# Kernel tuning notes

Hardware: AMD Instinct MI355X
Metric: run time of the kernel (lower is better)

The kernel has to match this reference:

```python
import jax, jax.numpy as jnp
import numpy as np

P = 4          # patch_size
LAM = 0.5      # init_lambda
B, C, H, W = 8, 96, 128, 128

def _dct_mat(N):
    # torch_dct unnormalized DCT-II matrix: D[k,n] = 2*cos(pi*(2n+1)k/(2N))
    n = np.arange(N)
    return 2.0 * np.cos(np.pi * (2.0 * n[None, :] + 1.0) * n[:, None] / (2.0 * N))

_D = jnp.asarray(_dct_mat(P), dtype=jnp.float32)
_Di = jnp.asarray(np.linalg.inv(_dct_mat(P)), dtype=jnp.float32)  # exact inverse -> idct(dct(x)) == x

def _dct2(x):
    # DCT-II over last two dims of [..., P, P]
    return jnp.einsum('ij,...jk,lk->...il', _D, x, _D)

def _idct2(x):
    return jnp.einsum('ij,...jk,lk->...il', _Di, x, _Di)

def _conv3x3(x, w, b):
    y = jax.lax.conv_general_dilated(x, w, (1, 1), 'SAME',
                                     dimension_numbers=('NCHW', 'OIHW', 'NCHW'))
    return y + b[None, :, None, None]

def setup_inputs() -> dict:
    key = jax.random.key(0)
    ks = jax.random.split(key, 5)
    std = 1.0 / np.sqrt(C * 9)
    return {
        'input1': jax.random.normal(ks[0], (B, C, H, W), jnp.float32),
        'input2': jax.random.normal(ks[1], (B, C, H, W), jnp.float32),
        'wq': jax.random.normal(ks[2], (C, C, 3, 3), jnp.float32) * std,
        'bq': jnp.zeros((C,), jnp.float32),
        'wk': jax.random.normal(ks[3], (C, C, 3, 3), jnp.float32) * std,
        'bk': jnp.zeros((C,), jnp.float32),
        'wv': jax.random.normal(ks[4], (C, C, 3, 3), jnp.float32) * std,
        'bv': jnp.zeros((C,), jnp.float32),
        'temperature': jnp.ones((1, 1), jnp.float32),
    }

def reference(input1, input2, wq, bq, wk, bk, wv, bv, temperature):
    b, c, h, w = input1.shape
    F_Q = _conv3x3(input1, wq, bq)
    F_K = _conv3x3(input1, wk, bk)
    F_V = _conv3x3(input2, wv, bv)
    hp, wp = h // P, w // P
    # 'b c (h p1) (w p2) -> b c h w p1 p2'
    to_patch = lambda x: x.reshape(b, c, hp, P, wp, P).transpose(0, 1, 2, 4, 3, 5)
    fft_Q = _dct2(to_patch(F_Q))          # [b,c,hp,wp,P,P]
    fft_K = _dct2(to_patch(F_K))
    F1 = jnp.matmul(fft_Q, fft_K)         # per-patch PxP matmul
    L = hp * wp * P * P                   # == h*w
    F1f = F1.reshape(b, c, L)
    Fq = fft_Q.reshape(b, c, L)
    Fk = fft_K.reshape(b, c, L)
    # channel-channel attention: [b,c,L] @ [b,L,c] -> [b,c,c]
    attn = jnp.einsum('bil,bjl->bij', Fq, Fk) * temperature[0, 0]
    attn = jax.nn.softmax(attn, axis=-1)
    Fcfr = jnp.einsum('bij,bjl->bil', attn, F1f).reshape(b, c, hp, wp, P, P)
    Fcfr_out = _idct2(Fcfr)
    # 'b c h w p1 p2 -> b c (h p1) (w p2)'
    Fcfrout = Fcfr_out.transpose(0, 1, 2, 4, 3, 5).reshape(b, c, h, w)
    out1 = jnp.matmul(Fcfrout, F_V)       # batched HxW matmul (H==W)
    Fdfr = F_V - out1 * LAM
    return jnp.matmul(Fcfrout, F_Q) + Fdfr
```

## Files before the change

### kernel.cpp

```cpp
#include <hip/hip_runtime.h>

typedef unsigned short u16;
typedef unsigned int u32;
typedef __bf16 bf16x8 __attribute__((ext_vector_type(8)));
typedef float f32x4 __attribute__((ext_vector_type(4)));
typedef int i32x4 __attribute__((ext_vector_type(4)));

#define BATCH 8
#define CH 96
#define HWSZ 16384
#define PADP (130*130*96)

#define OFF_FQ     0ULL
#define OFF_FK     50331648ULL
#define OFF_GT     50331648ULL
#define OFF_FVN    75497472ULL
#define OFF_PAD1H  100663296ULL
#define OFF_F1W    100663296ULL
#define OFF_PART   126621696ULL
#define OFF_PAD1L  126621696ULL
#define OFF_PAD2   152580096ULL
#define OFF_FCFR   152580096ULL
#define OFF_FVB    178538496ULL
#define OFF_ATTNB  203704320ULL
#define OFF_WQK    203851776ULL
#define OFF_WV     204515328ULL
#define WS_NEED    204681216ULL

__device__ __forceinline__ u16 f2bf(float f) {
    u32 u = __builtin_bit_cast(u32, f);
    u += 0x7fffu + ((u >> 16) & 1u);
    return (u16)(u >> 16);
}
__device__ __forceinline__ float bf2f(u16 h) {
    u32 u = ((u32)h) << 16;
    return __builtin_bit_cast(float, u);
}
__device__ __forceinline__ f32x4 mfma16(i32x4 a, i32x4 b, f32x4 c) {
    return __builtin_amdgcn_mfma_f32_16x16x32_bf16(
        __builtin_bit_cast(bf16x8, a), __builtin_bit_cast(bf16x8, b), c, 0, 0, 0);
}
__device__ __forceinline__ void gl_lds16(const u16* g, u16* l) {
    __builtin_amdgcn_global_load_lds(
        (const __attribute__((address_space(1))) unsigned int*)g,
        (__attribute__((address_space(3))) unsigned int*)l, 16, 0, 0);
}

__global__ __launch_bounds__(256) void k_diag(float* __restrict__ out, int n, float val) {
    for (int i = blockIdx.x * 256 + threadIdx.x; i < n; i += gridDim.x * 256) out[i] = val;
}

__global__ __launch_bounds__(256) void k_zhalo(u16* __restrict__ p) {
    size_t base = (size_t)blockIdx.x * PADP;
    for (int i = threadIdx.x; i < 130 * 96; i += 256) {
        p[base + i] = 0;
        p[base + (size_t)129 * 130 * 96 + i] = 0;
    }
    for (int i = threadIdx.x; i < 128 * 2 * 96; i += 256) {
        int row = i / 192, k = i - row * 192;
        int x = (k < 96) ? 0 : 129, c = (k < 96) ? k : k - 96;
        p[base + ((size_t)(row + 1) * 130 + x) * 96 + c] = 0;
    }
}

__global__ __launch_bounds__(256) void k_trans_split(const float* __restrict__ src,
        u16* __restrict__ dh, u16* __restrict__ dl) {
    __shared__ float tile[96][129];
    int b = blockIdx.x >> 7, y = blockIdx.x & 127;
    const float* s = src + (size_t)b * CH * HWSZ + (size_t)y * 128;
    for (int idx = threadIdx.x; idx < CH * 128; idx += 256) {
        int c = idx >> 7, x = idx & 127;
        tile[c][x] = s[(size_t)c * HWSZ + x];
    }
    __syncthreads();
    size_t obase = ((size_t)(b * 130 + y + 1) * 130 + 1) * 96;
    for (int idx = threadIdx.x; idx < 128 * CH; idx += 256) {
        int x = idx / CH, c = idx - x * CH;
        float v = tile[c][x];
        u16 h = f2bf(v);
        dh[obase + idx] = h;
        if (dl) dl[obase + idx] = f2bf(v - bf2f(h));
    }
}

__global__ __launch_bounds__(128) void k_weights_all(const float* __restrict__ wq,
        const float* __restrict__ wk, const float* __restrict__ wv,
        u16* __restrict__ dqk, u16* __restrict__ dv) {
    int co = blockIdx.x;
    if (co < 192) {
        const float* w = (co < 96) ? wq : wk;
        int cs = (co < 96) ? co : co - 96;
        for (int idx = threadIdx.x; idx < 864; idx += 128) {
            int tap = idx / 96, ci = idx - tap * 96;
            int cic = ci >> 5, g = (ci >> 3) & 3, c7 = ci & 7;
            float v = w[((size_t)cs * 96 + ci) * 9 + tap];
            u16 h = f2bf(v), lo = f2bf(v - bf2f(h));
            size_t s = (size_t)(cic * 9 + tap);
            dqk[(((s * 2 + 0) * 4 + g) * 192 + co) * 8 + c7] = h;
            dqk[(((s * 2 + 1) * 4 + g) * 192 + co) * 8 + c7] = lo;
        }
    } else {
        int cs = co - 192;
        for (int idx = threadIdx.x; idx < 864; idx += 128) {
            int tap = idx / 96, ci = idx - tap * 96;
            int cic = ci >> 5, g = (ci >> 3) & 3, c7 = ci & 7;
            float v = wv[((size_t)cs * 96 + ci) * 9 + tap];
            size_t s = (size_t)(cic * 9 + tap);
            dv[((s * 4 + g) * 96 + cs) * 8 + c7] = f2bf(v);
        }
    }
}

__global__ __launch_bounds__(512, 4) void k_convqk6(
        const u16* __restrict__ ph, const u16* __restrict__ pl,
        const u16* __restrict__ wqk,
        const float* __restrict__ bq, const float* __restrict__ bk,
        float* __restrict__ fq, float* __restrict__ fk) {
    __shared__ u16 wbuf[2][12288];
    const int tid = threadIdx.x;
    const int wg = ((blockIdx.x & 7) << 7) | (blockIdx.x >> 3);
    const int b = wg >> 7, y = wg & 127;
    const int w = tid >> 6, lane = tid & 63, l15 = lane & 15, g = lane >> 4;
    const int wx = w & 3, wc = w >> 2;
    f32x4 acc[2][6];
#pragma unroll
    for (int mf = 0; mf < 2; mf++)
#pragma unroll
        for (int f = 0; f < 6; f++) acc[mf][f] = (f32x4){0.f, 0.f, 0.f, 0.f};

    {
#pragma unroll
        for (int j = 0; j < 3; j++)
            gl_lds16(wqk + (size_t)(tid + j * 512) * 8, &wbuf[0][(size_t)(tid + j * 512) * 8]);
    }
    i32x4 ah0, ah1, al0, al1;
    {
        size_t ab = ((size_t)(b * 130 + y) * 130 + (wx * 32 + l15)) * 96 + g * 8;
        ah0 = *(const i32x4*)(ph + ab);
        ah1 = *(const i32x4*)(ph + ab + 16 * 96);
        al0 = *(const i32x4*)(pl + ab);
        al1 = *(const i32x4*)(pl + ab + 16 * 96);
    }
    __syncthreads();
    for (int s = 0; s < 27; s++) {
        const int cur = s & 1;
        i32x4 nh0, nh1, nl0, nl1;
        if (s + 1 < 27) {
            const u16* src = wqk + (size_t)(s + 1) * 12288;
#pragma unroll
            for (int j = 0; j < 3; j++)
                gl_lds16(src + (size_t)(tid + j * 512) * 8, &wbuf[cur ^ 1][(size_t)(tid + j * 512) * 8]);
            const int s1 = s + 1;
            const int cic1 = s1 / 9, tap1 = s1 - cic1 * 9;
            const int dy1 = tap1 / 3 - 1, dx1 = tap1 - (tap1 / 3) * 3 - 1;
            size_t ab = ((size_t)(b * 130 + y + 1 + dy1) * 130 + (wx * 32 + l15 + 1 + dx1)) * 96
                      + cic1 * 32 + g * 8;
            nh0 = *(const i32x4*)(ph + ab);
            nh1 = *(const i32x4*)(ph + ab + 16 * 96);
            nl0 = *(const i32x4*)(pl + ab);
            nl1 = *(const i32x4*)(pl + ab + 16 * 96);
        }
#pragma unroll
        for (int f = 0; f < 6; f++) {
            const int cob = wc * 96 + f * 16 + l15;
            i32x4 bh = *(const i32x4*)(&wbuf[cur][((0 + g) * 192 + cob) * 8]);
            i32x4 bl = *(const i32x4*)(&wbuf[cur][((4 + g) * 192 + cob) * 8]);
            acc[0][f] = mfma16(ah0, bh, acc[0][f]);
            acc[0][f] = mfma16(ah0, bl, acc[0][f]);
            acc[0][f] = mfma16(al0, bh, acc[0][f]);
            acc[1][f] = mfma16(ah1, bh, acc[1][f]);
            acc[1][f] = mfma16(ah1, bl, acc[1][f]);
            acc[1][f] = mfma16(al1, bh, acc[1][f]);
        }
        __syncthreads();
        if (s + 1 < 27) { ah0 = nh0; ah1 = nh1; al0 = nl0; al1 = nl1; }
    }
    const float* bias = wc ? bk : bq;
    float* op = wc ? fk : fq;
#pragma unroll
    for (int f = 0; f < 6; f++) {
        const int co = f * 16 + l15;
        const float bb = bias[co];
#pragma unroll
        for (int mf = 0; mf < 2; mf++) {
            const int xp = wx * 32 + mf * 16 + g * 4;
#pragma unroll
            for (int r = 0; r < 4; r++)
                op[((size_t)((b * 128 + y) * 128 + xp + r)) * 96 + co] = acc[mf][f][r] + bb;
        }
    }
}

__global__ __launch_bounds__(512, 4) void k_convv6(
        const u16* __restrict__ p2, const u16* __restrict__ wv,
        const float* __restrict__ bv, u16* __restrict__ fvb) {
    __shared__ u16 vbuf[2][3072];
    const int tid = threadIdx.x;
    const int wg = ((blockIdx.x & 7) << 7) | (blockIdx.x >> 3);
    const int b = wg >> 7, y = wg & 127;
    const int w = tid >> 6, lane = tid & 63, l15 = lane & 15, g = lane >> 4;
    const int wx = w & 3, wc = w >> 2;
    f32x4 acc[2][3];
#pragma unroll
    for (int mf = 0; mf < 2; mf++)
#pragma unroll
        for (int f = 0; f < 3; f++) acc[mf][f] = (f32x4){0.f, 0.f, 0.f, 0.f};
    if (tid < 384)
        gl_lds16(wv + (size_t)tid * 8, &vbuf[0][(size_t)tid * 8]);
    i32x4 ah0, ah1;
    {
        size_t ab = ((size_t)(b * 130 + y) * 130 + (wx * 32 + l15)) * 96 + g * 8;
        ah0 = *(const i32x4*)(p2 + ab);
        ah1 = *(const i32x4*)(p2 + ab + 16 * 96);
    }
    __syncthreads();
    for (int s = 0; s < 27; s++) {
        const int cur = s & 1;
        i32x4 nh0, nh1;
        if (s + 1 < 27) {
            if (tid < 384)
                gl_lds16(wv + (size_t)(s + 1) * 3072 + (size_t)tid * 8, &vbuf[cur ^ 1][(size_t)tid * 8]);
            const int s1 = s + 1;
            const int cic1 = s1 / 9, tap1 = s1 - cic1 * 9;
            const int dy1 = tap1 / 3 - 1, dx1 = tap1 - (tap1 / 3) * 3 - 1;
            size_t ab = ((size_t)(b * 130 + y + 1 + dy1) * 130 + (wx * 32 + l15 + 1 + dx1)) * 96
                      + cic1 * 32 + g * 8;
            nh0 = *(const i32x4*)(p2 + ab);
            nh1 = *(const i32x4*)(p2 + ab + 16 * 96);
        }
#pragma unroll
        for (int f = 0; f < 3; f++) {
            const int cof = wc * 48 + f * 16 + l15;
            i32x4 bfr = *(const i32x4*)(&vbuf[cur][(g * 96 + cof) * 8]);
            acc[0][f] = mfma16(ah0, bfr, acc[0][f]);
            acc[1][f] = mfma16(ah1, bfr, acc[1][f]);
        }
        __syncthreads();
        if (s + 1 < 27) { ah0 = nh0; ah1 = nh1; }
    }
#pragma unroll
    for (int f = 0; f < 3; f++) {
        const int co = wc * 48 + f * 16 + l15;
        const float bb = bv[co];
#pragma unroll
        for (int mf = 0; mf < 2; mf++) {
            const int xp = wx * 32 + mf * 16 + g * 4;
#pragma unroll
            for (int r = 0; r < 4; r++)
                fvb[((size_t)((b * 128 + y) * 128 + xp + r)) * 96 + co] = f2bf(acc[mf][f][r] + bb);
        }
    }
}

__global__ __launch_bounds__(256) void k_pattn(
        const float* __restrict__ fq, const float* __restrict__ fk,
        u16* __restrict__ f1w, float* __restrict__ part) {
    __shared__ float qs[96 * 129];
    __shared__ float ks[96 * 129];
    int blk = blockIdx.x;
    int b = blk >> 7, ys = (blk >> 2) & 31, xq = blk & 3;
    int y0 = ys * 4, x0 = xq * 32;
    for (int idx = threadIdx.x; idx < 3072; idx += 256) {
        int p = idx / 24, c0 = (idx - p * 24) * 4;
        int ry = p >> 5, rx = p & 31;
        size_t off = ((size_t)((b * 128 + y0 + ry) * 128 + x0 + rx)) * 96 + c0;
        f32x4 qv = *(const f32x4*)(fq + off);
        f32x4 kv = *(const f32x4*)(fk + off);
#pragma unroll
        for (int u = 0; u < 4; u++) {
            qs[(c0 + u) * 129 + p] = qv[u];
            ks[(c0 + u) * 129 + p] = kv[u];
        }
    }
    __syncthreads();
#pragma unroll
    for (int it = 0; it < 3; it++) {
        int item = threadIdx.x + it * 256;
        int j = item / 96, c = item - j * 96;
        float A[4][4], Bm[4][4];
#pragma unroll
        for (int r = 0; r < 4; r++)
#pragma unroll
            for (int m = 0; m < 4; m++) {
                A[r][m] = qs[c * 129 + r * 32 + j * 4 + m];
                Bm[r][m] = ks[c * 129 + r * 32 + j * 4 + m];
            }
        float rsB[4], csB[4], rsA[4], tot = 0.f;
#pragma unroll
        for (int r = 0; r < 4; r++) {
            rsB[r] = Bm[r][0] + Bm[r][1] + Bm[r][2] + Bm[r][3];
            rsA[r] = A[r][0] + A[r][1] + A[r][2] + A[r][3];
            tot += rsB[r];
        }
#pragma unroll
        for (int m = 0; m < 4; m++) csB[m] = Bm[0][m] + Bm[1][m] + Bm[2][m] + Bm[3][m];
#pragma unroll
        for (int r = 0; r < 4; r++)
#pragma unroll
            for (int m = 0; m < 4; m++) {
                float ab = A[r][0] * Bm[0][m] + A[r][1] * Bm[1][m]
                         + A[r][2] * Bm[2][m] + A[r][3] * Bm[3][m];
                f1w[((size_t)((b * 128 + y0 + r) * 128 + x0 + j * 4 + m)) * 96 + c]
                    = f2bf(8.f * ab + 2.f * rsA[r] * csB[m]);
            }
#pragma unroll
        for (int r = 0; r < 4; r++)
#pragma unroll
            for (int m = 0; m < 4; m++)
                ks[c * 129 + r * 32 + j * 4 + m]
                    = 64.f * Bm[r][m] + 16.f * (rsB[r] + csB[m]) + 4.f * tot;
    }
    __syncthreads();
    int tx = threadIdx.x & 15, ty = threadIdx.x >> 4;
    double accD[6][6];
#pragma unroll
    for (int a = 0; a < 6; a++)
#pragma unroll
        for (int bb = 0; bb < 6; bb++) accD[a][bb] = 0.0;
#pragma unroll
    for (int ch = 0; ch < 2; ch++) {
        float acc[6][6];
#pragma unroll
        for (int a = 0; a < 6; a++)
#pragma unroll
            for (int bb = 0; bb < 6; bb++) acc[a][bb] = 0.f;
        for (int l = ch * 64; l < ch * 64 + 64; l++) {
            float qv[6], kv[6];
#pragma unroll
            for (int a = 0; a < 6; a++) qv[a] = qs[(ty + 16 * a) * 129 + l];
#pragma unroll
            for (int bb = 0; bb < 6; bb++) kv[bb] = ks[(tx + 16 * bb) * 129 + l];
#pragma unroll
            for (int a = 0; a < 6; a++)
#pragma unroll
                for (int bb = 0; bb < 6; bb++) acc[a][bb] += qv[a] * kv[bb];
        }
#pragma unroll
        for (int a = 0; a < 6; a++)
#pragma unroll
            for (int bb = 0; bb < 6; bb++) accD[a][bb] += (double)acc[a][bb];
    }
    int s128 = ys * 4 + xq;
#pragma unroll
    for (int a = 0; a < 6; a++)
#pragma unroll
        for (int bb = 0; bb < 6; bb++)
            part[((size_t)((b * 128 + s128) * 96 + ty + 16 * a)) * 96 + tx + 16 * bb]
                = (float)accD[a][bb];
}

__global__ __launch_bounds__(128) void k_softmax(
        const float* __restrict__ part, const float* __restrict__ temp,
        u16* __restrict__ attnb) {
    __shared__ float red[128];
    int b = blockIdx.x / 96, i2 = blockIdx.x - b * 96;
    int j2 = threadIdx.x;
    float v = 0.f;
    if (j2 < 96) {
        double vd = 0.0;
        for (int s = 0; s < 128; s++)
            vd += (double)part[((size_t)((b * 128 + s) * 96 + i2)) * 96 + j2];
        v = (float)vd * temp[0];
    }
    red[j2] = (j2 < 96) ? v : -3.4e38f;
    __syncthreads();
    for (int off = 64; off >= 1; off >>= 1) {
        if (j2 < off) red[j2] = fmaxf(red[j2], red[j2 + off]);
        __syncthreads();
    }
    float mx = red[0];
    __syncthreads();
    float e = (j2 < 96) ? expf(v - mx) : 0.f;
    red[j2] = e;
    __syncthreads();
    for (int off = 64; off >= 1; off >>= 1) {
        if (j2 < off) red[j2] += red[j2 + off];
        __syncthreads();
    }
    float sum = red[0];
    if (j2 < 96) attnb[((size_t)(b * 96) + i2) * 96 + j2] = f2bf(e / sum);
}

__global__ __launch_bounds__(256) void k_gprep(
        const float* __restrict__ fqn, const u16* __restrict__ fvb,
        u16* __restrict__ gt, u16* __restrict__ fvn) {
    __shared__ u16 lg[8 * 32 * 33];
    __shared__ u16 lv[8 * 32 * 33];
    int blk = blockIdx.x;
    int b = blk / 192;
    int r = blk - b * 192;
    int yt = r / 48; r -= yt * 48;
    int xt = r / 12; int cc = r - xt * 12;
    int y0 = yt * 32, x0 = xt * 32, c0 = cc * 8;
    for (int idx = threadIdx.x; idx < 8192; idx += 256) {
        int pix = idx >> 3, cl = idx & 7;
        int yy = pix >> 5, xx = pix & 31;
        size_t off = ((size_t)((b * 128 + y0 + yy) * 128 + x0 + xx)) * 96 + c0 + cl;
        float q = fqn[off];
        float v = bf2f(fvb[off]);
        int la = (cl * 32 + yy) * 33 + xx;
        lg[la] = f2bf(q - 0.5f * v);
        lv[la] = f2bf(v);
    }
    __syncthreads();
    for (int idx = threadIdx.x; idx < 8192; idx += 256) {
        int yy = idx & 31, xl = (idx >> 5) & 31, cl = idx >> 10;
        gt[((size_t)((b * 96 + c0 + cl) * 128 + x0 + xl)) * 128 + y0 + yy] = lg[(cl * 32 + yy) * 33 + xl];
    }
    for (int idx = threadIdx.x; idx < 8192; idx += 256) {
        int xx = idx & 31, yl = (idx >> 5) & 31, cl = idx >> 10;
        fvn[((size_t)((b * 96 + c0 + cl) * 128 + y0 + yl)) * 128 + x0 + xx] = lv[(cl * 32 + yl) * 33 + xx];
    }
}

__global__ __launch_bounds__(256) void k_fcfr2(
        const u16* __restrict__ attnb, const u16* __restrict__ f1w,
        u16* __restrict__ fc) {
    int b = blockIdx.x >> 6, pc = blockIdx.x & 63;
    int lane = threadIdx.x & 63, wv_ = threadIdx.x >> 6;
    int l15 = lane & 15, g = lane >> 4;
    int pbase = pc * 256 + wv_ * 64;
    f32x4 acc[6][4];
#pragma unroll
    for (int m = 0; m < 6; m++)
#pragma unroll
        for (int n = 0; n < 4; n++) acc[m][n] = (f32x4){0.f, 0.f, 0.f, 0.f};
#pragma unroll
    for (int ks = 0; ks < 3; ks++) {
        int k0 = ks * 32 + g * 8;
        i32x4 afr[6];
#pragma unroll
        for (int m = 0; m < 6; m++)
            afr[m] = *(const i32x4*)(attnb + ((size_t)(b * 96 + m * 16 + l15)) * 96 + k0);
#pragma unroll
        for (int n = 0; n < 4; n++) {
            i32x4 bfr = *(const i32x4*)(f1w + ((size_t)(b * 16384 + pbase + n * 16 + l15)) * 96 + k0);
#pragma unroll
            for (int m = 0; m < 6; m++)
                acc[m][n] = mfma16(afr[m], bfr, acc[m][n]);
        }
    }
#pragma unroll
    for (int m = 0; m < 6; m++)
#pragma unroll
        for (int n = 0; n < 4; n++)
#pragma unroll
            for (int r = 0; r < 4; r++) {
                int i2 = m * 16 + g * 4 + r;
                int pix = pbase + n * 16 + l15;
                fc[((size_t)(b * 96 + i2)) * HWSZ + pix] = f2bf(acc[m][n][r]);
            }
}

__global__ __launch_bounds__(256) void k_final(
        const u16* __restrict__ fc, const u16* __restrict__ gt,
        const u16* __restrict__ fvn, float* __restrict__ out) {
    int b = blockIdx.x / 96, c = blockIdx.x - b * 96;
    int lane = threadIdx.x & 63, wv_ = threadIdx.x >> 6;
    int l15 = lane & 15, g = lane >> 4;
    const u16* A = fc + ((size_t)(b * 96 + c)) * HWSZ;
    const u16* Bm = gt + ((size_t)(b * 96 + c)) * HWSZ;
    f32x4 acc[2][8];
#pragma unroll
    for (int mf = 0; mf < 2; mf++)
#pragma unroll
        for (int nf = 0; nf < 8; nf++) acc[mf][nf] = (f32x4){0.f, 0.f, 0.f, 0.f};
#pragma unroll
    for (int kc = 0; kc < 4; kc++) {
        int k0 = kc * 32 + g * 8;
        i32x4 af[2];
#pragma unroll
        for (int mf = 0; mf < 2; mf++)
            af[mf] = *(const i32x4*)(A + (size_t)(wv_ * 32 + mf * 16 + l15) * 128 + k0);
#pragma unroll
        for (int nf = 0; nf < 8; nf++) {
            i32x4 bf = *(const i32x4*)(Bm + (size_t)(nf * 16 + l15) * 128 + k0);
#pragma unroll
            for (int mf = 0; mf < 2; mf++)
                acc[mf][nf] = mfma16(af[mf], bf, acc[mf][nf]);
        }
    }
    const u16* V = fvn + ((size_t)(b * 96 + c)) * HWSZ;
    float* O = out + ((size_t)(b * 96 + c)) * HWSZ;
#pragma unroll
    for (int mf = 0; mf < 2; mf++)
#pragma unroll
        for (int nf = 0; nf < 8; nf++)
#pragma unroll
            for (int r = 0; r < 4; r++) {
                int y = wv_ * 32 + mf * 16 + g * 4 + r;
                int x = nf * 16 + l15;
                O[y * 128 + x] = acc[mf][nf][r] + bf2f(V[y * 128 + x]);
            }
}

extern "C" void kernel_launch(void* const* d_in, const int* in_sizes, int n_in,
                              void* d_out, int out_size, void* d_ws, size_t ws_size,
                              hipStream_t stream) {
    (void)in_sizes; (void)n_in;
    if (ws_size < (size_t)WS_NEED) {
        k_diag<<<2048, 256, 0, stream>>>((float*)d_out, out_size, (float)(ws_size >> 10));
        return;
    }
    const float* in1 = (const float*)d_in[0];
    const float* in2 = (const float*)d_in[1];
    const float* wq  = (const float*)d_in[2];
    const float* bq  = (const float*)d_in[3];
    const float* wk  = (const float*)d_in[4];
    const float* bk  = (const float*)d_in[5];
    const float* wv  = (const float*)d_in[6];
    const float* bv  = (const float*)d_in[7];
    const float* temp = (const float*)d_in[8];
    char* ws = (char*)d_ws;
    float* FQ   = (float*)(ws + OFF_FQ);
    float* FK   = (float*)(ws + OFF_FK);
    u16*  GT    = (u16*)(ws + OFF_GT);
    u16*  FVN   = (u16*)(ws + OFF_FVN);
    u16*  PAD1H = (u16*)(ws + OFF_PAD1H);
    u16*  PAD1L = (u16*)(ws + OFF_PAD1L);
    u16*  PAD2  = (u16*)(ws + OFF_PAD2);
    u16*  F1W   = (u16*)(ws + OFF_F1W);
    float* PART = (float*)(ws + OFF_PART);
    u16*  FCFR  = (u16*)(ws + OFF_FCFR);
    u16*  FVB   = (u16*)(ws + OFF_FVB);
    u16*  ATTNB = (u16*)(ws + OFF_ATTNB);
    u16*  WQK   = (u16*)(ws + OFF_WQK);
    u16*  WV    = (u16*)(ws + OFF_WV);

    k_zhalo<<<24, 256, 0, stream>>>(PAD1H);
    k_trans_split<<<1024, 256, 0, stream>>>(in1, PAD1H, PAD1L);
    k_trans_split<<<1024, 256, 0, stream>>>(in2, PAD2, nullptr);
    k_weights_all<<<288, 128, 0, stream>>>(wq, wk, wv, WQK, WV);
    k_convqk6<<<1024, 512, 0, stream>>>(PAD1H, PAD1L, WQK, bq, bk, FQ, FK);
    k_convv6<<<1024, 512, 0, stream>>>(PAD2, WV, bv, FVB);
    k_pattn<<<1024, 256, 0, stream>>>(FQ, FK, F1W, PART);
    k_softmax<<<768, 128, 0, stream>>>(PART, temp, ATTNB);
    k_gprep<<<1536, 256, 0, stream>>>(FQ, FVB, GT, FVN);
    k_fcfr2<<<512, 256, 0, stream>>>(ATTNB, F1W, FCFR);
    k_final<<<768, 256, 0, stream>>>(FCFR, GT, FVN, (float*)d_out);
}
```

Before: 409.7 us.

## Split QK conv across two kernel variants and halve pattn shared memory

The Q/K convolution is split into two launches over batch halves. The first half keeps the old wave tiling; the second uses a new variant where each wave covers 64 pixels by 48 output channels, reusing each weight fragment across four M-fragments. The patch-attention kernel now stages its 128-pixel tile in two 64-pixel chunks, roughly halving LDS use so more blocks can be resident, at the cost of extra barriers. Splitting the conv looks like an A/B comparison of the two tilings, and it adds a launch plus more register pressure in the new variant.

```diff
diff --git a/kernel.cpp b/kernel.cpp
--- a/kernel.cpp
+++ b/kernel.cpp
@@ -111,15 +111,15 @@
     }
 }
 
-__global__ __launch_bounds__(512, 4) void k_convqk6(
+__global__ __launch_bounds__(512, 4) void k_convqk6h(
         const u16* __restrict__ ph, const u16* __restrict__ pl,
         const u16* __restrict__ wqk,
         const float* __restrict__ bq, const float* __restrict__ bk,
-        float* __restrict__ fq, float* __restrict__ fk) {
+        float* __restrict__ fq, float* __restrict__ fk, int bbase) {
     __shared__ u16 wbuf[2][12288];
     const int tid = threadIdx.x;
-    const int wg = ((blockIdx.x & 7) << 7) | (blockIdx.x >> 3);
-    const int b = wg >> 7, y = wg & 127;
+    const int wg = ((blockIdx.x & 7) << 6) | (blockIdx.x >> 3);
+    const int b = bbase + (wg >> 7), y = wg & 127;
     const int w = tid >> 6, lane = tid & 63, l15 = lane & 15, g = lane >> 4;
     const int wx = w & 3, wc = w >> 2;
     f32x4 acc[2][6];
@@ -127,7 +127,6 @@
     for (int mf = 0; mf < 2; mf++)
 #pragma unroll
         for (int f = 0; f < 6; f++) acc[mf][f] = (f32x4){0.f, 0.f, 0.f, 0.f};
-
     {
 #pragma unroll
         for (int j = 0; j < 3; j++)
@@ -184,6 +183,91 @@
 #pragma unroll
         for (int mf = 0; mf < 2; mf++) {
             const int xp = wx * 32 + mf * 16 + g * 4;
+#pragma unroll
+            for (int r = 0; r < 4; r++)
+                op[((size_t)((b * 128 + y) * 128 + xp + r)) * 96 + co] = acc[mf][f][r] + bb;
+        }
+    }
+}
+
+__global__ __launch_bounds__(512, 4) void k_convqk7h(
+        const u16* __restrict__ ph, const u16* __restrict__ pl,
+        const u16* __restrict__ wqk,
+        const float* __restrict__ bq, const float* __restrict__ bk,
+        float* __restrict__ fq, float* __restrict__ fk, int bbase) {
+    __shared__ u16 wbuf[2][12288];
+    const int tid = threadIdx.x;
+    const int wg = ((blockIdx.x & 7) << 6) | (blockIdx.x >> 3);
+    const int b = bbase + (wg >> 7), y = wg & 127;
+    const int w = tid >> 6, lane = tid & 63, l15 = lane & 15, g = lane >> 4;
+    const int qk = w >> 2, coh = (w >> 1) & 1, xh = w & 1;
+    const int cob = qk * 96 + coh * 48;
+    f32x4 acc[4][3];
+#pragma unroll
+    for (int mf = 0; mf < 4; mf++)
+#pragma unroll
+        for (int f = 0; f < 3; f++) acc[mf][f] = (f32x4){0.f, 0.f, 0.f, 0.f};
+    {
+#pragma unroll
+        for (int j = 0; j < 3; j++)
+            gl_lds16(wqk + (size_t)(tid + j * 512) * 8, &wbuf[0][(size_t)(tid + j * 512) * 8]);
+    }
+    i32x4 ah[4], al[4];
+    {
+        size_t ab = ((size_t)(b * 130 + y) * 130 + (xh * 64 + l15)) * 96 + g * 8;
+#pragma unroll
+        for (int mf = 0; mf < 4; mf++) {
+            ah[mf] = *(const i32x4*)(ph + ab + (size_t)mf * 16 * 96);
+            al[mf] = *(const i32x4*)(pl + ab + (size_t)mf * 16 * 96);
+        }
+    }
+    __syncthreads();
+    for (int s = 0; s < 27; s++) {
+        const int cur = s & 1;
+        i32x4 nah[4], nal[4];
+        if (s + 1 < 27) {
+            const u16* src = wqk + (size_t)(s + 1) * 12288;
+#pragma unroll
+            for (int j = 0; j < 3; j++)
+                gl_lds16(src + (size_t)(tid + j * 512) * 8, &wbuf[cur ^ 1][(size_t)(tid + j * 512) * 8]);
+            const int s1 = s + 1;
+            const int cic1 = s1 / 9, tap1 = s1 - cic1 * 9;
+            const int dy1 = tap1 / 3 - 1, dx1 = tap1 - (tap1 / 3) * 3 - 1;
+            size_t ab1 = ((size_t)(b * 130 + y + 1 + dy1) * 130 + (xh * 64 + l15 + 1 + dx1)) * 96
+                       + cic1 * 32 + g * 8;
+#pragma unroll
+            for (int mf = 0; mf < 4; mf++) {
+                nah[mf] = *(const i32x4*)(ph + ab1 + (size_t)mf * 16 * 96);
+                nal[mf] = *(const i32x4*)(pl + ab1 + (size_t)mf * 16 * 96);
+            }
+        }
+#pragma unroll
+        for (int f = 0; f < 3; f++) {
+            const int cw = cob + f * 16 + l15;
+            i32x4 bh = *(const i32x4*)(&wbuf[cur][((0 + g) * 192 + cw) * 8]);
+            i32x4 bl = *(const i32x4*)(&wbuf[cur][((4 + g) * 192 + cw) * 8]);
+#pragma unroll
+            for (int mf = 0; mf < 4; mf++) {
+                acc[mf][f] = mfma16(ah[mf], bh, acc[mf][f]);
+                acc[mf][f] = mfma16(ah[mf], bl, acc[mf][f]);
+                acc[mf][f] = mfma16(al[mf], bh, acc[mf][f]);
+            }
+        }
+        __syncthreads();
+        if (s + 1 < 27) {
+#pragma unroll
+            for (int mf = 0; mf < 4; mf++) { ah[mf] = nah[mf]; al[mf] = nal[mf]; }
+        }
+    }
+    const float* bias = qk ? bk : bq;
+    float* op = qk ? fk : fq;
+#pragma unroll
+    for (int f = 0; f < 3; f++) {
+        const int co = coh * 48 + f * 16 + l15;
+        const float bb = bias[co];
+#pragma unroll
+        for (int mf = 0; mf < 4; mf++) {
+            const int xp = xh * 64 + mf * 16 + g * 4;
 #pragma unroll
             for (int r = 0; r < 4; r++)
                 op[((size_t)((b * 128 + y) * 128 + xp + r)) * 96 + co] = acc[mf][f][r] + bb;
@@ -252,65 +336,14 @@
     }
 }
 
-__global__ __launch_bounds__(256) void k_pattn(
+__global__ __launch_bounds__(256) void k_pattn2(
         const float* __restrict__ fq, const float* __restrict__ fk,
         u16* __restrict__ f1w, float* __restrict__ part) {
-    __shared__ float qs[96 * 129];
-    __shared__ float ks[96 * 129];
+    __shared__ float qs[96 * 65];
+    __shared__ float ks[96 * 65];
     int blk = blockIdx.x;
     int b = blk >> 7, ys = (blk >> 2) & 31, xq = blk & 3;
     int y0 = ys * 4, x0 = xq * 32;
-    for (int idx = threadIdx.x; idx < 3072; idx += 256) {
-        int p = idx / 24, c0 = (idx - p * 24) * 4;
-        int ry = p >> 5, rx = p & 31;
-        size_t off = ((size_t)((b * 128 + y0 + ry) * 128 + x0 + rx)) * 96 + c0;
-        f32x4 qv = *(const f32x4*)(fq + off);
-        f32x4 kv = *(const f32x4*)(fk + off);
-#pragma unroll
-        for (int u = 0; u < 4; u++) {
-            qs[(c0 + u) * 129 + p] = qv[u];
-            ks[(c0 + u) * 129 + p] = kv[u];
-        }
-    }
-    __syncthreads();
-#pragma unroll
-    for (int it = 0; it < 3; it++) {
-        int item = threadIdx.x + it * 256;
-        int j = item / 96, c = item - j * 96;
-        float A[4][4], Bm[4][4];
-#pragma unroll
-        for (int r = 0; r < 4; r++)
-#pragma unroll
-            for (int m = 0; m < 4; m++) {
-                A[r][m] = qs[c * 129 + r * 32 + j * 4 + m];
-                Bm[r][m] = ks[c * 129 + r * 32 + j * 4 + m];
-            }
-        float rsB[4], csB[4], rsA[4], tot = 0.f;
-#pragma unroll
-        for (int r = 0; r < 4; r++) {
-            rsB[r] = Bm[r][0] + Bm[r][1] + Bm[r][2] + Bm[r][3];
-            rsA[r] = A[r][0] + A[r][1] + A[r][2] + A[r][3];
-            tot += rsB[r];
-        }
-#pragma unroll
-        for (int m = 0; m < 4; m++) csB[m] = Bm[0][m] + Bm[1][m] + Bm[2][m] + Bm[3][m];
-#pragma unroll
-        for (int r = 0; r < 4; r++)
-#pragma unroll
-            for (int m = 0; m < 4; m++) {
-                float ab = A[r][0] * Bm[0][m] + A[r][1] * Bm[1][m]
-                         + A[r][2] * Bm[2][m] + A[r][3] * Bm[3][m];
-                f1w[((size_t)((b * 128 + y0 + r) * 128 + x0 + j * 4 + m)) * 96 + c]
-                    = f2bf(8.f * ab + 2.f * rsA[r] * csB[m]);
-            }
-#pragma unroll
-        for (int r = 0; r < 4; r++)
-#pragma unroll
-            for (int m = 0; m < 4; m++)
-                ks[c * 129 + r * 32 + j * 4 + m]
-                    = 64.f * Bm[r][m] + 16.f * (rsB[r] + csB[m]) + 4.f * tot;
-    }
-    __syncthreads();
     int tx = threadIdx.x & 15, ty = threadIdx.x >> 4;
     double accD[6][6];
 #pragma unroll
@@ -318,18 +351,67 @@
 #pragma unroll
         for (int bb = 0; bb < 6; bb++) accD[a][bb] = 0.0;
 #pragma unroll
-    for (int ch = 0; ch < 2; ch++) {
+    for (int cx = 0; cx < 2; cx++) {
+        for (int idx = threadIdx.x; idx < 1536; idx += 256) {
+            int p = idx / 24, c0 = (idx - p * 24) * 4;
+            int ry = p >> 4, rx = p & 15;
+            size_t off = ((size_t)((b * 128 + y0 + ry) * 128 + x0 + cx * 16 + rx)) * 96 + c0;
+            f32x4 qv = *(const f32x4*)(fq + off);
+            f32x4 kv = *(const f32x4*)(fk + off);
+#pragma unroll
+            for (int u = 0; u < 4; u++) {
+                qs[(c0 + u) * 65 + p] = qv[u];
+                ks[(c0 + u) * 65 + p] = kv[u];
+            }
+        }
+        __syncthreads();
+        for (int item = threadIdx.x; item < 384; item += 256) {
+            int j = item / 96, c = item - j * 96;
+            float A[4][4], Bm[4][4];
+#pragma unroll
+            for (int r = 0; r < 4; r++)
+#pragma unroll
+                for (int m = 0; m < 4; m++) {
+                    A[r][m] = qs[c * 65 + r * 16 + j * 4 + m];
+                    Bm[r][m] = ks[c * 65 + r * 16 + j * 4 + m];
+                }
+            float rsB[4], csB[4], rsA[4], tot = 0.f;
+#pragma unroll
+            for (int r = 0; r < 4; r++) {
+                rsB[r] = Bm[r][0] + Bm[r][1] + Bm[r][2] + Bm[r][3];
+                rsA[r] = A[r][0] + A[r][1] + A[r][2] + A[r][3];
+                tot += rsB[r];
+            }
+#pragma unroll
+            for (int m = 0; m < 4; m++) csB[m] = Bm[0][m] + Bm[1][m] + Bm[2][m] + Bm[3][m];
+#pragma unroll
+            for (int r = 0; r < 4; r++)
+#pragma unroll
+                for (int m = 0; m < 4; m++) {
+                    float ab = A[r][0] * Bm[0][m] + A[r][1] * Bm[1][m]
+                             + A[r][2] * Bm[2][m] + A[r][3] * Bm[3][m];
+                    f1w[((size_t)((b * 128 + y0 + r) * 128 + x0 + cx * 16 + j * 4 + m)) * 96 + c]
+                        = f2bf(8.f * ab + 2.f * rsA[r] * csB[m]);
+                }
+#pragma unroll
+            for (int r = 0; r < 4; r++)
+#pragma unroll
+                for (int m = 0; m < 4; m++)
+                    ks[c * 65 + r * 16 + j * 4 + m]
+                        = 64.f * Bm[r][m] + 16.f * (rsB[r] + csB[m]) + 4.f * tot;
+        }
+        __syncthreads();
         float acc[6][6];
 #pragma unroll
         for (int a = 0; a < 6; a++)
 #pragma unroll
             for (int bb = 0; bb < 6; bb++) acc[a][bb] = 0.f;
-        for (int l = ch * 64; l < ch * 64 + 64; l++) {
+        for (int l = 0; l < 64; l++) {
             float qv[6], kv[6];
 #pragma unroll
-            for (int a = 0; a < 6; a++) qv[a] = qs[(ty + 16 * a) * 129 + l];
-#pragma unroll
-            for (int bb = 0; bb < 6; bb++) kv[bb] = ks[(tx + 16 * bb) * 129 + l];
+            for (int a = 0; a < 6; a++) qv[a] = qs[(ty + 16 * a) * 65 + l];
+#pragma unroll
+            for (int bb = 0; bb < 6; bb++) kv[bb] = ks[(tx + 16 * bb) * 65 + l];
 #pragma unroll
             for (int a = 0; a < 6; a++)
 #pragma unroll
@@ -339,6 +421,7 @@
         for (int a = 0; a < 6; a++)
 #pragma unroll
             for (int bb = 0; bb < 6; bb++) accD[a][bb] += (double)acc[a][bb];
+        __syncthreads();
     }
     int s128 = ys * 4 + xq;
 #pragma unroll
@@ -531,9 +614,10 @@
     k_trans_split<<<1024, 256, 0, stream>>>(in1, PAD1H, PAD1L);
     k_trans_split<<<1024, 256, 0, stream>>>(in2, PAD2, nullptr);
     k_weights_all<<<288, 128, 0, stream>>>(wq, wk, wv, WQK, WV);
-    k_convqk6<<<1024, 512, 0, stream>>>(PAD1H, PAD1L, WQK, bq, bk, FQ, FK);
+    k_convqk6h<<<512, 512, 0, stream>>>(PAD1H, PAD1L, WQK, bq, bk, FQ, FK, 0);
+    k_convqk7h<<<512, 512, 0, stream>>>(PAD1H, PAD1L, WQK, bq, bk, FQ, FK, 4);
     k_convv6<<<1024, 512, 0, stream>>>(PAD2, WV, bv, FVB);
-    k_pattn<<<1024, 256, 0, stream>>>(FQ, FK, F1W, PART);
+    k_pattn2<<<1024, 256, 0, stream>>>(FQ, FK, F1W, PART);
     k_softmax<<<768, 128, 0, stream>>>(PART, temp, ATTNB);
     k_gprep<<<1536, 256, 0, stream>>>(FQ, FVB, GT, FVN);
     k_fcfr2<<<512, 256, 0, stream>>>(ATTNB, F1W, FCFR);
```

New measurement: 413.6 us. About the same (+0.9%).

## Split Q/K conv across blocks with LDS input slab; halve pattn LDS footprint

Applied to the files above, without the earlier changes.

The Q/K convolution is split so that each block computes only Q or only K for one row, which doubles the grid. The weight layout is reorganised per Q/K half. The three padded input rows (hi and lo planes) for each channel chunk are staged into shared memory once and reused across all 9 taps, replacing per-tap global loads. Separately, the patch-attention kernel processes its 32-pixel tile in two 16-pixel halves, halving its shared memory use to allow more resident blocks. The cost is extra syncs and a larger LDS slab in the conv.

```diff
diff --git a/kernel.cpp b/kernel.cpp
--- a/kernel.cpp
+++ b/kernel.cpp
@@ -88,16 +88,17 @@
         u16* __restrict__ dqk, u16* __restrict__ dv) {
     int co = blockIdx.x;
     if (co < 192) {
-        const float* w = (co < 96) ? wq : wk;
-        int cs = (co < 96) ? co : co - 96;
+        const int qk = (co < 96) ? 0 : 1;
+        const float* w = qk ? wk : wq;
+        int cs = co - qk * 96;
         for (int idx = threadIdx.x; idx < 864; idx += 128) {
             int tap = idx / 96, ci = idx - tap * 96;
             int cic = ci >> 5, g = (ci >> 3) & 3, c7 = ci & 7;
             float v = w[((size_t)cs * 96 + ci) * 9 + tap];
             u16 h = f2bf(v), lo = f2bf(v - bf2f(h));
-            size_t s = (size_t)(cic * 9 + tap);
-            dqk[(((s * 2 + 0) * 4 + g) * 192 + co) * 8 + c7] = h;
-            dqk[(((s * 2 + 1) * 4 + g) * 192 + co) * 8 + c7] = lo;
+            size_t s = (size_t)(qk * 27 + cic * 9 + tap);
+            dqk[(((s * 2 + 0) * 4 + g) * 96 + cs) * 8 + c7] = h;
+            dqk[(((s * 2 + 1) * 4 + g) * 96 + cs) * 8 + c7] = lo;
         }
     } else {
         int cs = co - 192;
@@ -111,75 +112,93 @@
     }
 }
 
-__global__ __launch_bounds__(512, 4) void k_convqk6(
+__global__ __launch_bounds__(512, 4) void k_convqk8(
         const u16* __restrict__ ph, const u16* __restrict__ pl,
         const u16* __restrict__ wqk,
         const float* __restrict__ bq, const float* __restrict__ bk,
         float* __restrict__ fq, float* __restrict__ fk) {
-    __shared__ u16 wbuf[2][12288];
+    __shared__ __attribute__((aligned(16))) u16 aslab[3120 * 8];
+    __shared__ __attribute__((aligned(16))) u16 wbuf[2][6144];
     const int tid = threadIdx.x;
-    const int wg = ((blockIdx.x & 7) << 7) | (blockIdx.x >> 3);
-    const int b = wg >> 7, y = wg & 127;
+    const int wg = ((blockIdx.x & 7) << 8) | (blockIdx.x >> 3);
+    const int b = wg >> 8, y = (wg >> 1) & 127, qk = wg & 1;
     const int w = tid >> 6, lane = tid & 63, l15 = lane & 15, g = lane >> 4;
     const int wx = w & 3, wc = w >> 2;
-    f32x4 acc[2][6];
+    f32x4 acc[2][3];
 #pragma unroll
     for (int mf = 0; mf < 2; mf++)
 #pragma unroll
-        for (int f = 0; f < 6; f++) acc[mf][f] = (f32x4){0.f, 0.f, 0.f, 0.f};
-
-    {
-#pragma unroll
-        for (int j = 0; j < 3; j++)
-            gl_lds16(wqk + (size_t)(tid + j * 512) * 8, &wbuf[0][(size_t)(tid + j * 512) * 8]);
-    }
-    i32x4 ah0, ah1, al0, al1;
-    {
-        size_t ab = ((size_t)(b * 130 + y) * 130 + (wx * 32 + l15)) * 96 + g * 8;
-        ah0 = *(const i32x4*)(ph + ab);
-        ah1 = *(const i32x4*)(ph + ab + 16 * 96);
-        al0 = *(const i32x4*)(pl + ab);
-        al1 = *(const i32x4*)(pl + ab + 16 * 96);
-    }
-    __syncthreads();
-    for (int s = 0; s < 27; s++) {
-        const int cur = s & 1;
-        i32x4 nh0, nh1, nl0, nl1;
-        if (s + 1 < 27) {
-            const u16* src = wqk + (size_t)(s + 1) * 12288;
-#pragma unroll
-            for (int j = 0; j < 3; j++)
-                gl_lds16(src + (size_t)(tid + j * 512) * 8, &wbuf[cur ^ 1][(size_t)(tid + j * 512) * 8]);
-            const int s1 = s + 1;
-            const int cic1 = s1 / 9, tap1 = s1 - cic1 * 9;
-            const int dy1 = tap1 / 3 - 1, dx1 = tap1 - (tap1 / 3) * 3 - 1;
-            size_t ab = ((size_t)(b * 130 + y + 1 + dy1) * 130 + (wx * 32 + l15 + 1 + dx1)) * 96
-                      + cic1 * 32 + g * 8;
-            nh0 = *(const i32x4*)(ph + ab);
-            nh1 = *(const i32x4*)(ph + ab + 16 * 96);
-            nl0 = *(const i32x4*)(pl + ab);
-            nl1 = *(const i32x4*)(pl + ab + 16 * 96);
-        }
-#pragma unroll
-        for (int f = 0; f < 6; f++) {
-            const int cob = wc * 96 + f * 16 + l15;
-            i32x4 bh = *(const i32x4*)(&wbuf[cur][((0 + g) * 192 + cob) * 8]);
-            i32x4 bl = *(const i32x4*)(&wbuf[cur][((4 + g) * 192 + cob) * 8]);
-            acc[0][f] = mfma16(ah0, bh, acc[0][f]);
-            acc[0][f] = mfma16(ah0, bl, acc[0][f]);
-            acc[0][f] = mfma16(al0, bh, acc[0][f]);
-            acc[1][f] = mfma16(ah1, bh, acc[1][f]);
-            acc[1][f] = mfma16(ah1, bl, acc[1][f]);
-            acc[1][f] = mfma16(al1, bh, acc[1][f]);
-        }
-        __syncthreads();
-        if (s + 1 < 27) { ah0 = nh0; ah1 = nh1; al0 = nl0; al1 = nl1; }
-    }
-    const float* bias = wc ? bk : bq;
-    float* op = wc ? fk : fq;
-#pragma unroll
-    for (int f = 0; f < 6; f++) {
-        const int co = f * 16 + l15;
+        for (int f = 0; f < 3; f++) acc[mf][f] = (f32x4){0.f, 0.f, 0.f, 0.f};
+
+    const u16* wbase = wqk + (size_t)qk * 27 * 6144;
+
+    for (int cic = 0; cic < 3; cic++) {
+#pragma unroll
+        for (int k = 0; k < 6; k++) {
+            int idx = tid + k * 512;
+            int pr = idx / 130, x = idx - pr * 130;
+            int g4 = pr & 3, prow = pr >> 2;
+            int plane = (prow >= 3) ? 1 : 0, row = prow - plane * 3;
+            const u16* src = (plane ? pl : ph)
+                + ((size_t)((b * 130 + y + row) * 130 + x)) * 96 + cic * 32 + g4 * 8;
+            gl_lds16(src, aslab + (size_t)idx * 8);
+        }
+        if (tid < 48) {
+            int idx = 3072 + tid;
+            int pr = idx / 130, x = idx - pr * 130;
+            int g4 = pr & 3, prow = pr >> 2;
+            int plane = (prow >= 3) ? 1 : 0, row = prow - plane * 3;
+            const u16* src = (plane ? pl : ph)
+                + ((size_t)((b * 130 + y + row) * 130 + x)) * 96 + cic * 32 + g4 * 8;
+            i32x4 v = *(const i32x4*)src;
+            *(i32x4*)(aslab + (size_t)idx * 8) = v;
+        }
+        if (cic == 0) {
+            gl_lds16(wbase + (size_t)tid * 8, &wbuf[0][0] + (size_t)tid * 8);
+            if (tid < 256)
+                gl_lds16(wbase + (size_t)(512 + tid) * 8, &wbuf[0][0] + (size_t)(512 + tid) * 8);
+        }
+        __syncthreads();
+
+        for (int tap = 0; tap < 9; tap++) {
+            const int s = cic * 9 + tap;
+            const int cur = s & 1;
+            if (s + 1 < 27) {
+                const u16* src = wbase + (size_t)(s + 1) * 6144;
+                u16* dst = &wbuf[cur ^ 1][0];
+                gl_lds16(src + (size_t)tid * 8, dst + (size_t)tid * 8);
+                if (tid < 256)
+                    gl_lds16(src + (size_t)(512 + tid) * 8, dst + (size_t)(512 + tid) * 8);
+            }
+            const int dy = tap / 3, dx = tap - dy * 3;
+            const int px = wx * 32 + l15 + dx;
+            const int base0 = ((dy * 4 + g) * 130 + px) * 8;
+            const int base1 = base0 + 12 * 130 * 8;
+            i32x4 ah0 = *(const i32x4*)(aslab + base0);
+            i32x4 ah1 = *(const i32x4*)(aslab + base0 + 16 * 8);
+            i32x4 al0 = *(const i32x4*)(aslab + base1);
+            i32x4 al1 = *(const i32x4*)(aslab + base1 + 16 * 8);
+            const u16* wb = &wbuf[cur][0];
+#pragma unroll
+            for (int f = 0; f < 3; f++) {
+                const int co = wc * 48 + f * 16 + l15;
+                i32x4 bh = *(const i32x4*)(wb + (size_t)((0 + g) * 96 + co) * 8);
+                i32x4 bl = *(const i32x4*)(wb + (size_t)((4 + g) * 96 + co) * 8);
+                acc[0][f] = mfma16(ah0, bh, acc[0][f]);
+                acc[0][f] = mfma16(ah0, bl, acc[0][f]);
+                acc[0][f] = mfma16(al0, bh, acc[0][f]);
+                acc[1][f] = mfma16(ah1, bh, acc[1][f]);
+                acc[1][f] = mfma16(ah1, bl, acc[1][f]);
+                acc[1][f] = mfma16(al1, bh, acc[1][f]);
+            }
+            __syncthreads();
+        }
+    }
+    const float* bias = qk ? bk : bq;
+    float* op = qk ? fk : fq;
+#pragma unroll
+    for (int f = 0; f < 3; f++) {
+        const int co = wc * 48 + f * 16 + l15;
         const float bb = bias[co];
 #pragma unroll
         for (int mf = 0; mf < 2; mf++) {
@@ -252,65 +271,14 @@
     }
 }
 
-__global__ __launch_bounds__(256) void k_pattn(
+__global__ __launch_bounds__(256) void k_pattn2(
         const float* __restrict__ fq, const float* __restrict__ fk,
         u16* __restrict__ f1w, float* __restrict__ part) {
-    __shared__ float qs[96 * 129];
-    __shared__ float ks[96 * 129];
+    __shared__ float qs[96 * 65];
+    __shared__ float ks[96 * 65];
     int blk = blockIdx.x;
     int b = blk >> 7, ys = (blk >> 2) & 31, xq = blk & 3;
     int y0 = ys * 4, x0 = xq * 32;
-    for (int idx = threadIdx.x; idx < 3072; idx += 256) {
-        int p = idx / 24, c0 = (idx - p * 24) * 4;
-        int ry = p >> 5, rx = p & 31;
-        size_t off = ((size_t)((b * 128 + y0 + ry) * 128 + x0 + rx)) * 96 + c0;
-        f32x4 qv = *(const f32x4*)(fq + off);
-        f32x4 kv = *(const f32x4*)(fk + off);
-#pragma unroll
-        for (int u = 0; u < 4; u++) {
-            qs[(c0 + u) * 129 + p] = qv[u];
-            ks[(c0 + u) * 129 + p] = kv[u];
-        }
-    }
-    __syncthreads();
-#pragma unroll
-    for (int it = 0; it < 3; it++) {
-        int item = threadIdx.x + it * 256;
-        int j = item / 96, c = item - j * 96;
-        float A[4][4], Bm[4][4];
-#pragma unroll
-        for (int r = 0; r < 4; r++)
-#pragma unroll
-            for (int m = 0; m < 4; m++) {
-                A[r][m] = qs[c * 129 + r * 32 + j * 4 + m];
-                Bm[r][m] = ks[c * 129 + r * 32 + j * 4 + m];
-            }
-        float rsB[4], csB[4], rsA[4], tot = 0.f;
-#pragma unroll
-        for (int r = 0; r < 4; r++) {
-            rsB[r] = Bm[r][0] + Bm[r][1] + Bm[r][2] + Bm[r][3];
-            rsA[r] = A[r][0] + A[r][1] + A[r][2] + A[r][3];
-            tot += rsB[r];
-        }
-#pragma unroll
-        for (int m = 0; m < 4; m++) csB[m] = Bm[0][m] + Bm[1][m] + Bm[2][m] + Bm[3][m];
-#pragma unroll
-        for (int r = 0; r < 4; r++)
-#pragma unroll
-            for (int m = 0; m < 4; m++) {
-                float ab = A[r][0] * Bm[0][m] + A[r][1] * Bm[1][m]
-                         + A[r][2] * Bm[2][m] + A[r][3] * Bm[3][m];
-                f1w[((size_t)((b * 128 + y0 + r) * 128 + x0 + j * 4 + m)) * 96 + c]
-                    = f2bf(8.f * ab + 2.f * rsA[r] * csB[m]);
-            }
-#pragma unroll
-        for (int r = 0; r < 4; r++)
-#pragma unroll
-            for (int m = 0; m < 4; m++)
-                ks[c * 129 + r * 32 + j * 4 + m]
-                    = 64.f * Bm[r][m] + 16.f * (rsB[r] + csB[m]) + 4.f * tot;
-    }
-    __syncthreads();
     int tx = threadIdx.x & 15, ty = threadIdx.x >> 4;
     double accD[6][6];
 #pragma unroll
@@ -318,18 +286,67 @@
 #pragma unroll
         for (int bb = 0; bb < 6; bb++) accD[a][bb] = 0.0;
 #pragma unroll
-    for (int ch = 0; ch < 2; ch++) {
+    for (int cx = 0; cx < 2; cx++) {
+        for (int idx = threadIdx.x; idx < 1536; idx += 256) {
+            int p = idx / 24, c0 = (idx - p * 24) * 4;
+            int ry = p >> 4, rx = p & 15;
+            size_t off = ((size_t)((b * 128 + y0 + ry) * 128 + x0 + cx * 16 + rx)) * 96 + c0;
+            f32x4 qv = *(const f32x4*)(fq + off);
+            f32x4 kv = *(const f32x4*)(fk + off);
+#pragma unroll
+            for (int u = 0; u < 4; u++) {
+                qs[(c0 + u) * 65 + p] = qv[u];
+                ks[(c0 + u) * 65 + p] = kv[u];
+            }
+        }
+        __syncthreads();
+        for (int item = threadIdx.x; item < 384; item += 256) {
+            int j = item / 96, c = item - j * 96;
+            float A[4][4], Bm[4][4];
+#pragma unroll
+            for (int r = 0; r < 4; r++)
+#pragma unroll
+                for (int m = 0; m < 4; m++) {
+                    A[r][m] = qs[c * 65 + r * 16 + j * 4 + m];
+                    Bm[r][m] = ks[c * 65 + r * 16 + j * 4 + m];
+                }
+            float rsB[4], csB[4], rsA[4], tot = 0.f;
+#pragma unroll
+            for (int r = 0; r < 4; r++) {
+                rsB[r] = Bm[r][0] + Bm[r][1] + Bm[r][2] + Bm[r][3];
+                rsA[r] = A[r][0] + A[r][1] + A[r][2] + A[r][3];
+                tot += rsB[r];
+            }
+#pragma unroll
+            for (int m = 0; m < 4; m++) csB[m] = Bm[0][m] + Bm[1][m] + Bm[2][m] + Bm[3][m];
+#pragma unroll
+            for (int r = 0; r < 4; r++)
+#pragma unroll
+                for (int m = 0; m < 4; m++) {
+                    float ab = A[r][0] * Bm[0][m] + A[r][1] * Bm[1][m]
+                             + A[r][2] * Bm[2][m] + A[r][3] * Bm[3][m];
+                    f1w[((size_t)((b * 128 + y0 + r) * 128 + x0 + cx * 16 + j * 4 + m)) * 96 + c]
+                        = f2bf(8.f * ab + 2.f * rsA[r] * csB[m]);
+                }
+#pragma unroll
+            for (int r = 0; r < 4; r++)
+#pragma unroll
+                for (int m = 0; m < 4; m++)
+                    ks[c * 65 + r * 16 + j * 4 + m]
+                        = 64.f * Bm[r][m] + 16.f * (rsB[r] + csB[m]) + 4.f * tot;
+        }
+        __syncthreads();
         float acc[6][6];
 #pragma unroll
         for (int a = 0; a < 6; a++)
 #pragma unroll
             for (int bb = 0; bb < 6; bb++) acc[a][bb] = 0.f;
-        for (int l = ch * 64; l < ch * 64 + 64; l++) {
+        for (int l = 0; l < 64; l++) {
             float qv[6], kv[6];
 #pragma unroll
-            for (int a = 0; a < 6; a++) qv[a] = qs[(ty + 16 * a) * 129 + l];
-#pragma unroll
-            for (int bb = 0; bb < 6; bb++) kv[bb] = ks[(tx + 16 * bb) * 129 + l];
+            for (int a = 0; a < 6; a++) qv[a] = qs[(ty + 16 * a) * 65 + l];
+#pragma unroll
+            for (int bb = 0; bb < 6; bb++) kv[bb] = ks[(tx + 16 * bb) * 65 + l];
 #pragma unroll
             for (int a = 0; a < 6; a++)
 #pragma unroll
@@ -339,6 +356,7 @@
         for (int a = 0; a < 6; a++)
 #pragma unroll
             for (int bb = 0; bb < 6; bb++) accD[a][bb] += (double)acc[a][bb];
+        __syncthreads();
     }
     int s128 = ys * 4 + xq;
 #pragma unroll
@@ -531,9 +549,9 @@
     k_trans_split<<<1024, 256, 0, stream>>>(in1, PAD1H, PAD1L);
     k_trans_split<<<1024, 256, 0, stream>>>(in2, PAD2, nullptr);
     k_weights_all<<<288, 128, 0, stream>>>(wq, wk, wv, WQK, WV);
-    k_convqk6<<<1024, 512, 0, stream>>>(PAD1H, PAD1L, WQK, bq, bk, FQ, FK);
+    k_convqk8<<<2048, 512, 0, stream>>>(PAD1H, PAD1L, WQK, bq, bk, FQ, FK);
     k_convv6<<<1024, 512, 0, stream>>>(PAD2, WV, bv, FVB);
-    k_pattn<<<1024, 256, 0, stream>>>(FQ, FK, F1W, PART);
+    k_pattn2<<<1024, 256, 0, stream>>>(FQ, FK, F1W, PART);
     k_softmax<<<768, 128, 0, stream>>>(PART, temp, ATTNB);
     k_gprep<<<1536, 256, 0, stream>>>(FQ, FVB, GT, FVN);
     k_fcfr2<<<512, 256, 0, stream>>>(ATTNB, F1W, FCFR);
```

Result: faster. 392.3 us (-4.3%).
